# Optimization experiments

Hardware: AMD Instinct MI355X
Metric: run time of the kernel (lower is better)

The kernel has to match this reference:

```python
import jax, jax.numpy as jnp
import numpy as np

ROT_DIM = 32  # rotary sub-dimension hardcoded in the original module


def apply_rope(x, rope):
    # x: [B, T, H, hd], rope: [T, ROT_DIM//2, 2]
    T = x.shape[1]
    rc = rope[:T][:, None]            # [T, 1, 16, 2]
    cos, sin = rc[..., 0], rc[..., 1]  # [T, 1, 16]
    x_rot, x_pass = x[..., :ROT_DIM], x[..., ROT_DIM:]
    x1, x2 = x_rot[..., :ROT_DIM // 2], x_rot[..., ROT_DIM // 2:]
    return jnp.concatenate([x1 * cos - x2 * sin, x2 * cos + x1 * sin, x_pass], axis=-1)


def setup_inputs() -> dict:
    key = jax.random.key(0)
    ks = jax.random.split(key, 6)
    B, T, C, H = 4, 1024, 2048, 32
    hd = C // H
    x = jax.random.normal(ks[0], (B, T, C), dtype=jnp.float32)
    mask = jnp.tril(jnp.ones((T, T), dtype=bool))  # causal, True = attend
    index = jnp.arange(T, dtype=jnp.int64) if jax.config.jax_enable_x64 else jnp.arange(T, dtype=jnp.int32)
    # realistic rotary cos/sin cache
    inv_freq = 1.0 / (10000.0 ** (np.arange(0, ROT_DIM, 2, dtype=np.float32) / ROT_DIM))
    ang = np.arange(T, dtype=np.float32)[:, None] * inv_freq[None, :]  # [T, 16]
    rope = jnp.asarray(np.stack([np.cos(ang), np.sin(ang)], axis=-1))   # [T, 16, 2]
    s = 1.0 / np.sqrt(C)
    Wqkv_w = jax.random.normal(ks[1], (3 * C, C), dtype=jnp.float32) * s
    Wqkv_b = jax.random.normal(ks[2], (3 * C,), dtype=jnp.float32) * 0.01
    out_w = jax.random.normal(ks[3], (C, C), dtype=jnp.float32) * s
    out_b = jax.random.normal(ks[4], (C,), dtype=jnp.float32) * 0.01
    k_cache = jnp.zeros((B, H, T, hd), dtype=jnp.float32)
    v_cache = jnp.zeros((B, H, T, hd), dtype=jnp.float32)
    return {"x": x, "mask": mask, "index": index, "rope": rope,
            "Wqkv_w": Wqkv_w, "Wqkv_b": Wqkv_b, "out_w": out_w, "out_b": out_b,
            "k_cache": k_cache, "v_cache": v_cache}


def reference(x, mask, index, rope, Wqkv_w, Wqkv_b, out_w, out_b, k_cache, v_cache):
    B, T, C = x.shape
    H = 32
    hd = C // H
    qkv = x @ Wqkv_w.T + Wqkv_b                 # [B, T, 3C]
    q, k, v = jnp.split(qkv, 3, axis=-1)
    q = q.reshape(B, T, H, hd)
    k = k.reshape(B, T, H, hd)
    v = v.reshape(B, T, H, hd)
    q = apply_rope(q, rope)
    k = apply_rope(k, rope)
    q = q.transpose(0, 2, 1, 3)                 # [B, H, T, hd]
    k = k.transpose(0, 2, 1, 3)
    v = v.transpose(0, 2, 1, 3)
    # KV-cache scatter update; index = arange(T) covers the full cache, so the
    # subsequent slice [:, :, :index[-1]+1] is the whole cache (static shape).
    k_full = k_cache.at[:, :, index].set(k)
    v_full = v_cache.at[:, :, index].set(v)
    scores = jnp.einsum('bhqd,bhkd->bhqk', q, k_full) / jnp.sqrt(jnp.asarray(hd, x.dtype))
    scores = jnp.where(mask, scores, jnp.finfo(x.dtype).min)
    attn = jax.nn.softmax(scores, axis=-1)
    ctx = jnp.einsum('bhqk,bhkd->bhqd', attn, v_full)
    ctx = ctx.transpose(0, 2, 1, 3).reshape(B, T, C)
    return ctx @ out_w.T + out_b
```

## Files before the change

kernel.cpp:

```cpp
#include <hip/hip_runtime.h>

typedef unsigned short u16;
typedef unsigned int u32;
typedef __bf16 bf16x8 __attribute__((ext_vector_type(8)));
typedef float floatx4 __attribute__((ext_vector_type(4)));
typedef u16 u16x4 __attribute__((ext_vector_type(4)));
typedef u16 u16x8 __attribute__((ext_vector_type(8)));
typedef u32 u32x2 __attribute__((ext_vector_type(2)));

#define B_ 4
#define T_ 1024
#define C_ 2048
#define H_ 32
#define HD_ 64

__device__ __forceinline__ float b2f(u16 u) {
    u32 x = ((u32)u) << 16;
    return __builtin_bit_cast(float, x);
}
__device__ __forceinline__ u16 f2b(float f) {
    u32 i = __builtin_bit_cast(u32, f);
    u32 r = (i + 0x7FFFu + ((i >> 16) & 1u)) >> 16;
    return (u16)r;
}
__device__ __forceinline__ u32 pack2(float a, float b) {
    const u32 ua = __builtin_bit_cast(u32, a) + 0x8000u;
    const u32 ub = __builtin_bit_cast(u32, b) + 0x8000u;
    return __builtin_amdgcn_perm(ub, ua, 0x07060302u);
}

#define GLOAD16(gp, lp) __builtin_amdgcn_global_load_lds( \
    (const __attribute__((address_space(1))) void*)(gp),  \
    (__attribute__((address_space(3))) void*)(lp), 16, 0, 0)

__global__ __launch_bounds__(256) void convert_bf16(const float* __restrict__ src,
                                                    u16* __restrict__ dst, int n4) {
    const int stride = gridDim.x * 256;
    for (int i = blockIdx.x * 256 + threadIdx.x; i < n4; i += stride) {
        const floatx4 v = *(const floatx4*)(src + (size_t)i * 4);
        const u32x2 h = {pack2(v.x, v.y), pack2(v.z, v.w)};
        *(u32x2*)(dst + (size_t)i * 4) = h;
    }
}

template <int MODE>
__global__ __launch_bounds__(256) void gemm_bt(const u16* __restrict__ A,
                                               const u16* __restrict__ W,
                                               const float* __restrict__ bias,
                                               const float* __restrict__ rope,
                                               void* __restrict__ o0v,
                                               u16* __restrict__ o1,
                                               u16* __restrict__ o2) {
    const int Kdim = 2048;
    __shared__ __align__(16) u16 As[128 * 64];
    __shared__ __align__(16) u16 Bs[128 * 64];

    const int tid = threadIdx.x;
    const int w = tid >> 6, lane = tid & 63;
    const int wr = w >> 1, wc = w & 1;
    const int quad = lane >> 4, l15 = lane & 15;
    const int mBase = blockIdx.y * 128, nBase = blockIdx.x * 128;

    floatx4 acc[4][4] = {};

    const int lrow = lane >> 3;
    const int lcol = ((lane & 7) ^ lrow) * 8;
    const u16* Ap = A + (size_t)(mBase + lrow) * Kdim + lcol;
    const u16* Wp = W + (size_t)(nBase + lrow) * Kdim + lcol;

    const int xk = l15 & 7;

    for (int k0 = 0; k0 < Kdim; k0 += 64) {
#pragma unroll
        for (int i = 0; i < 4; i++) {
            const int c = i * 4 + w;
            GLOAD16(Ap + (size_t)c * 8 * Kdim + k0, &As[c * 512]);
            GLOAD16(Wp + (size_t)c * 8 * Kdim + k0, &Bs[c * 512]);
        }
        __syncthreads();
#pragma unroll
        for (int ks = 0; ks < 64; ks += 32) {
            bf16x8 af[4], bfr[4];
#pragma unroll
            for (int i = 0; i < 4; i++) {
                const int co = (((ks >> 3) + quad) ^ xk) * 8;
                af[i] = *(const bf16x8*)&As[(wr * 64 + i * 16 + l15) * 64 + co];
            }
#pragma unroll
            for (int j = 0; j < 4; j++) {
                const int co = (((ks >> 3) + quad) ^ xk) * 8;
                bfr[j] = *(const bf16x8*)&Bs[(wc * 64 + j * 16 + l15) * 64 + co];
            }
#pragma unroll
            for (int i = 0; i < 4; i++)
#pragma unroll
                for (int j = 0; j < 4; j++)
                    acc[i][j] = __builtin_amdgcn_mfma_f32_16x16x32_bf16(af[i], bfr[j], acc[i][j], 0, 0, 0);
        }
        __syncthreads();
    }

    const int nq = nBase + wc * 64;
    float bv[4];
#pragma unroll
    for (int j = 0; j < 4; j++) bv[j] = bias[nq + j * 16 + l15];

    if (MODE == 0) {
        const int region = nq >> 11;
        const int h = (nq & 2047) >> 6;
        const int d = l15;
        u16* dst = (region == 0) ? (u16*)o0v : ((region == 1) ? o1 : o2);
#pragma unroll
        for (int i = 0; i < 4; i++) {
#pragma unroll
            for (int r = 0; r < 4; r++) {
                const int m = mBase + wr * 64 + i * 16 + quad * 4 + r;
                const int b = m >> 10, t = m & 1023;
                float v0 = acc[i][0][r] + bv[0];
                float v1 = acc[i][1][r] + bv[1];
                float v2 = acc[i][2][r] + bv[2];
                float v3 = acc[i][3][r] + bv[3];
                const size_t base = ((size_t)(b * H_ + h) * T_ + t) * HD_;
                if (region < 2) {
                    const float cz = rope[t * 32 + d * 2];
                    const float sz = rope[t * 32 + d * 2 + 1];
                    const float n0 = v0 * cz - v1 * sz;
                    const float n1 = v1 * cz + v0 * sz;
                    dst[base + d] = f2b(n0);
                    dst[base + 16 + d] = f2b(n1);
                } else {
                    dst[base + d] = f2b(v0);
                    dst[base + 16 + d] = f2b(v1);
                }
                dst[base + 32 + d] = f2b(v2);
                dst[base + 48 + d] = f2b(v3);
            }
        }
    } else {
        float* outf = (float*)o0v;
#pragma unroll
        for (int i = 0; i < 4; i++)
#pragma unroll
            for (int r = 0; r < 4; r++) {
                const int m = mBase + wr * 64 + i * 16 + quad * 4 + r;
                const size_t o = (size_t)m * 2048 + nq;
#pragma unroll
                for (int j = 0; j < 4; j++)
                    outf[o + j * 16 + l15] = acc[i][j][r] + bv[j];
            }
    }
}

#define VT_STR 72

__global__ __launch_bounds__(256) void attn_mfma(const u16* __restrict__ qT,
                                                 const u16* __restrict__ kT,
                                                 const u16* __restrict__ vT,
                                                 u16* __restrict__ ctx) {
    __shared__ __align__(16) u16 Vt[2][64 * VT_STR];
    __shared__ __align__(16) u16 Pt[4 * 16 * VT_STR];

    const int tid = threadIdx.x;
    const int w = tid >> 6, lane = tid & 63;
    const int quad = lane >> 4, l15 = lane & 15;
    const int bh = blockIdx.y;
    const size_t headBase = (size_t)bh * (T_ * HD_);

    u16* myPt = &Pt[w * 16 * VT_STR];
    const int vhd = tid & 63, vkb = tid >> 6;
    const float SC = 0.18033688011112042f;

    int gb = 0;
#pragma unroll 1
    for (int ti = 0; ti < 2; ti++) {
        const int qt = ti ? (15 - (int)blockIdx.x) : (int)blockIdx.x;

        bf16x8 qf[2];
        {
            const u16* qrow = qT + headBase + ((size_t)qt * 64 + w * 16 + l15) * HD_ + quad * 8;
            qf[0] = __builtin_bit_cast(bf16x8, *(const u16x8*)(qrow));
            qf[1] = __builtin_bit_cast(bf16x8, *(const u16x8*)(qrow + 32));
        }

        float m_i = -1e30f, l_i = 0.f;
        floatx4 oacc[4] = {};

        for (int kt = 0; kt <= qt; kt++) {
            const u16* kp = kT + headBase + (size_t)kt * 64 * HD_;
            const u16* vp = vT + headBase + (size_t)kt * 64 * HD_;

            u16 vreg[16];
#pragma unroll
            for (int c = 0; c < 16; c++)
                vreg[c] = vp[(vkb * 16 + c) * HD_ + vhd];

            floatx4 st[4] = {};
#pragma unroll
            for (int mi = 0; mi < 4; mi++) {
                const u16* krow = kp + (mi * 16 + l15) * HD_ + quad * 8;
                const bf16x8 kf0 = __builtin_bit_cast(bf16x8, *(const u16x8*)(krow));
                const bf16x8 kf1 = __builtin_bit_cast(bf16x8, *(const u16x8*)(krow + 32));
                st[mi] = __builtin_amdgcn_mfma_f32_16x16x32_bf16(kf0, qf[0], st[mi], 0, 0, 0);
                st[mi] = __builtin_amdgcn_mfma_f32_16x16x32_bf16(kf1, qf[1], st[mi], 0, 0, 0);
            }

            u16* vt = Vt[gb];
#pragma unroll
            for (int c4 = 0; c4 < 4; c4++) {
                const u16x4 vv = {vreg[c4 * 4], vreg[c4 * 4 + 1], vreg[c4 * 4 + 2], vreg[c4 * 4 + 3]};
                *(u16x4*)&vt[vhd * VT_STR + vkb * 16 + c4 * 4] = vv;
            }
            __syncthreads();

            float pmax = -1e30f;
#pragma unroll
            for (int mi = 0; mi < 4; mi++)
#pragma unroll
                for (int r = 0; r < 4; r++) {
                    float sv = st[mi][r] * SC;
                    if (kt == qt && (mi * 16 + quad * 4 + r) > (w * 16 + l15)) sv = -1e30f;
                    st[mi][r] = sv;
                    pmax = fmaxf(pmax, sv);
                }
            pmax = fmaxf(pmax, __shfl_xor(pmax, 16, 64));
            pmax = fmaxf(pmax, __shfl_xor(pmax, 32, 64));
            const float mnew = fmaxf(m_i, pmax);
            const float alpha = __builtin_amdgcn_exp2f(m_i - mnew);
            m_i = mnew;

            float psum = 0.f;
#pragma unroll
            for (int mi = 0; mi < 4; mi++) {
                float p[4];
#pragma unroll
                for (int r = 0; r < 4; r++) {
                    p[r] = __builtin_amdgcn_exp2f(st[mi][r] - mnew);
                    psum += p[r];
                }
                const u32x2 pk2 = {pack2(p[0], p[1]), pack2(p[2], p[3])};
                *(u32x2*)&myPt[l15 * VT_STR + mi * 16 + quad * 4] = pk2;
            }
            psum += __shfl_xor(psum, 16, 64);
            psum += __shfl_xor(psum, 32, 64);
            l_i = l_i * alpha + psum;

#pragma unroll
            for (int mi = 0; mi < 4; mi++) oacc[mi] *= alpha;

            bf16x8 pf[2];
            pf[0] = __builtin_bit_cast(bf16x8, *(const u16x8*)&myPt[l15 * VT_STR + quad * 8]);
            pf[1] = __builtin_bit_cast(bf16x8, *(const u16x8*)&myPt[l15 * VT_STR + 32 + quad * 8]);
#pragma unroll
            for (int mi = 0; mi < 4; mi++) {
                const bf16x8 vf0 = __builtin_bit_cast(bf16x8, *(const u16x8*)&vt[(mi * 16 + l15) * VT_STR + quad * 8]);
                const bf16x8 vf1 = __builtin_bit_cast(bf16x8, *(const u16x8*)&vt[(mi * 16 + l15) * VT_STR + 32 + quad * 8]);
                oacc[mi] = __builtin_amdgcn_mfma_f32_16x16x32_bf16(vf0, pf[0], oacc[mi], 0, 0, 0);
                oacc[mi] = __builtin_amdgcn_mfma_f32_16x16x32_bf16(vf1, pf[1], oacc[mi], 0, 0, 0);
            }
            gb ^= 1;
        }

        const float inv = 1.0f / l_i;
        const int b = bh >> 5, h = bh & 31;
        const int t = qt * 64 + w * 16 + l15;
        u16* cp = ctx + ((size_t)(b * T_ + t)) * C_ + h * HD_;
#pragma unroll
        for (int mi = 0; mi < 4; mi++) {
            const u16x4 ov = {f2b(oacc[mi][0] * inv), f2b(oacc[mi][1] * inv),
                              f2b(oacc[mi][2] * inv), f2b(oacc[mi][3] * inv)};
            *(u16x4*)(cp + mi * 16 + quad * 4) = ov;
        }
    }
}

extern "C" void kernel_launch(void* const* d_in, const int* in_sizes, int n_in,
                              void* d_out, int out_size, void* d_ws, size_t ws_size,
                              hipStream_t stream) {
    const float* x      = (const float*)d_in[0];
    const float* rope   = (const float*)d_in[3];
    const float* Wqkv_w = (const float*)d_in[4];
    const float* Wqkv_b = (const float*)d_in[5];
    const float* out_w  = (const float*)d_in[6];
    const float* out_b  = (const float*)d_in[7];
    float* out = (float*)d_out;

    const size_t headElems = (size_t)B_ * H_ * T_ * HD_;
    u16* xb    = (u16*)d_ws;
    u16* wqkvb = xb + headElems;
    u16* outwb = wqkvb + 12582912;
    u16* qTp   = outwb + 4194304;
    u16* kTp   = qTp + headElems;
    u16* vTp   = kTp + headElems;
    u16* ctx   = xb;

    convert_bf16<<<dim3(2048), 256, 0, stream>>>(x, xb, 2097152);
    convert_bf16<<<dim3(3072), 256, 0, stream>>>(Wqkv_w, wqkvb, 3145728);
    convert_bf16<<<dim3(1024), 256, 0, stream>>>(out_w, outwb, 1048576);

    gemm_bt<0><<<dim3(48, 32), 256, 0, stream>>>(xb, wqkvb, Wqkv_b, rope, qTp, kTp, vTp);
    attn_mfma<<<dim3(8, 128), 256, 0, stream>>>(qTp, kTp, vTp, ctx);
    gemm_bt<1><<<dim3(16, 32), 256, 0, stream>>>(ctx, outwb, out_b, rope, out, nullptr, nullptr);
}
```

Baseline: 433.6 us.

## Replace QKV GEMM with 256x256 double-buffered 8-wave pipelined kernel

Adds a new QKV projection kernel that uses 256x256 output tiles with 512 threads and double-buffered LDS staging. Global-to-LDS loads are interleaved with MFMA phases, guarded by explicit barriers, waitcnts and setprio, and blocks are remapped with a swizzle for L2 locality. Bias, rope and the head-split layout are kept in the epilogue. The aim is more data reuse per tile and overlap of memory with compute. In exchange it uses much more LDS (128KB) and registers, so occupancy drops, and the 384-block grid may leave the 256 CUs unevenly loaded.

```diff
diff --git a/kernel.cpp b/kernel.cpp
--- a/kernel.cpp
+++ b/kernel.cpp
@@ -33,6 +33,13 @@
     (const __attribute__((address_space(1))) void*)(gp),  \
     (__attribute__((address_space(3))) void*)(lp), 16, 0, 0)
 
+#define BAR()   __builtin_amdgcn_s_barrier()
+#define LGKM0() asm volatile("s_waitcnt lgkmcnt(0)" ::: "memory")
+#define VMW(n)  asm volatile("s_waitcnt vmcnt(" #n ")" ::: "memory")
+#define PRIO1() __builtin_amdgcn_s_setprio(1)
+#define PRIO0() __builtin_amdgcn_s_setprio(0)
+#define MFMA(a, b, c) __builtin_amdgcn_mfma_f32_16x16x32_bf16(a, b, c, 0, 0, 0)
+
 __global__ __launch_bounds__(256) void convert_bf16(const float* __restrict__ src,
                                                     u16* __restrict__ dst, int n4) {
     const int stride = gridDim.x * 256;
@@ -40,6 +47,169 @@
         const floatx4 v = *(const floatx4*)(src + (size_t)i * 4);
         const u32x2 h = {pack2(v.x, v.y), pack2(v.z, v.w)};
         *(u32x2*)(dst + (size_t)i * 4) = h;
+    }
+}
+
+#define HALFSTEP(BUF, STG, TS, VMN)                                           \
+  {                                                                           \
+    const u16* as = &As[BUF][0];                                              \
+    const u16* bs = &Bs[BUF][0];                                              \
+    u16* asw = &As[BUF][0];                                                   \
+    u16* bsw = &Bs[BUF][0];                                                   \
+    const u16* Apt = Abase + (size_t)(TS) * 64;                               \
+    const u16* Wpt = Wbase + (size_t)(TS) * 64;                               \
+    bf16x8 afr[4][2], bfr[4][2];                                              \
+                            \
+    _Pragma("unroll") for (int i = 0; i < 4; i++) {                           \
+      afr[i][0] = *(const bf16x8*)&as[aro + i * 1024 + co0];                  \
+      afr[i][1] = *(const bf16x8*)&as[aro + i * 1024 + co1];                  \
+    }                                                                         \
+    _Pragma("unroll") for (int j = 0; j < 2; j++) {                           \
+      bfr[j][0] = *(const bf16x8*)&bs[bro + j * 1024 + co0];                  \
+      bfr[j][1] = *(const bf16x8*)&bs[bro + j * 1024 + co1];                  \
+    }                                                                         \
+    BAR(); LGKM0(); PRIO1();                                                  \
+    _Pragma("unroll") for (int i = 0; i < 4; i++)                             \
+      _Pragma("unroll") for (int j = 0; j < 2; j++) {                         \
+        acc[i][j] = MFMA(afr[i][0], bfr[j][0], acc[i][j]);                    \
+        acc[i][j] = MFMA(afr[i][1], bfr[j][1], acc[i][j]);                    \
+      }                                                                       \
+    PRIO0(); BAR();                                                           \
+                 \
+    _Pragma("unroll") for (int j = 2; j < 4; j++) {                           \
+      bfr[j][0] = *(const bf16x8*)&bs[bro + j * 1024 + co0];                  \
+      bfr[j][1] = *(const bf16x8*)&bs[bro + j * 1024 + co1];                  \
+    }                                                                         \
+    if (STG) {                                                                \
+      GLOAD16(Apt, &asw[(w * 8) * 64]);                                       \
+      GLOAD16(Apt + (size_t)2 * 131072, &asw[(128 + w * 8) * 64]);            \
+    }                                                                         \
+    BAR(); LGKM0(); PRIO1();                                                  \
+    _Pragma("unroll") for (int i = 0; i < 4; i++)                             \
+      _Pragma("unroll") for (int j = 2; j < 4; j++) {                         \
+        acc[i][j] = MFMA(afr[i][0], bfr[j][0], acc[i][j]);                    \
+        acc[i][j] = MFMA(afr[i][1], bfr[j][1], acc[i][j]);                    \
+      }                                                                       \
+    PRIO0(); BAR();                                                           \
+                       \
+    _Pragma("unroll") for (int i = 0; i < 4; i++) {                           \
+      afr[i][0] = *(const bf16x8*)&as[aro + 4096 + i * 1024 + co0];           \
+      afr[i][1] = *(const bf16x8*)&as[aro + 4096 + i * 1024 + co1];           \
+    }                                                                         \
+    if (STG) {                                                                \
+      GLOAD16(Wpt, &bsw[(w * 8) * 64]);                                       \
+      GLOAD16(Wpt + (size_t)131072, &bsw[(64 + w * 8) * 64]);                 \
+    }                                                                         \
+    BAR(); LGKM0(); PRIO1();                                                  \
+    _Pragma("unroll") for (int i = 0; i < 4; i++)                             \
+      _Pragma("unroll") for (int j = 0; j < 2; j++) {                         \
+        acc[4 + i][j] = MFMA(afr[i][0], bfr[j][0], acc[4 + i][j]);            \
+        acc[4 + i][j] = MFMA(afr[i][1], bfr[j][1], acc[4 + i][j]);            \
+      }                                                                       \
+    PRIO0(); BAR();                                                           \
+            \
+    if (STG) {                                                                \
+      GLOAD16(Wpt + (size_t)2 * 131072, &bsw[(128 + w * 8) * 64]);            \
+      GLOAD16(Wpt + (size_t)3 * 131072, &bsw[(192 + w * 8) * 64]);            \
+      GLOAD16(Apt + (size_t)131072, &asw[(64 + w * 8) * 64]);                 \
+      GLOAD16(Apt + (size_t)3 * 131072, &asw[(192 + w * 8) * 64]);            \
+    }                                                                         \
+    BAR(); PRIO1();                                                           \
+    _Pragma("unroll") for (int i = 0; i < 4; i++)                             \
+      _Pragma("unroll") for (int j = 2; j < 4; j++) {                         \
+        acc[4 + i][j] = MFMA(afr[i][0], bfr[j][0], acc[4 + i][j]);            \
+        acc[4 + i][j] = MFMA(afr[i][1], bfr[j][1], acc[4 + i][j]);            \
+      }                                                                       \
+    PRIO0(); VMW(VMN); BAR();                                                 \
+  }
+
+__global__ __launch_bounds__(512) void gemm256_qkv(const u16* __restrict__ A,
+                                                   const u16* __restrict__ W,
+                                                   const float* __restrict__ bias,
+                                                   const float* __restrict__ rope,
+                                                   u16* __restrict__ oq,
+                                                   u16* __restrict__ ok,
+                                                   u16* __restrict__ ov) {
+    __shared__ __align__(16) u16 As[2][256 * 64];
+    __shared__ __align__(16) u16 Bs[2][256 * 64];
+
+    const int tid = threadIdx.x;
+    const int w = tid >> 6, lane = tid & 63;
+    const int quad = lane >> 4, l15 = lane & 15;
+    const int wr = w >> 2, wc = w & 3;
+
+    const int lin = blockIdx.y * 24 + blockIdx.x;
+    const int swz = (lin & 7) * 48 + (lin >> 3);
+    const int mBase = (swz & 15) * 256;
+    const int nBase = (swz >> 4) * 256;
+
+    const int srow = w * 8 + (lane >> 3);
+    const int scol = ((lane & 7) ^ (lane >> 3)) * 8;
+    const u16* Abase = A + (size_t)(mBase + srow) * 2048 + scol;
+    const u16* Wbase = W + (size_t)(nBase + srow) * 2048 + scol;
+
+    const int xk = l15 & 7;
+    const int co0 = ((0 * 4 + quad) ^ xk) * 8;
+    const int co1 = ((1 * 4 + quad) ^ xk) * 8;
+    const int aro = (wr * 128 + l15) * 64;
+    const int bro = (wc * 64 + l15) * 64;
+
+    floatx4 acc[8][4] = {};
+
+#pragma unroll
+    for (int u = 0; u < 4; u++) {
+        GLOAD16(Abase + (size_t)u * 131072, &As[0][(u * 64 + w * 8) * 64]);
+        GLOAD16(Wbase + (size_t)u * 131072, &Bs[0][(u * 64 + w * 8) * 64]);
+    }
+#pragma unroll
+    for (int u = 0; u < 4; u++) {
+        GLOAD16(Abase + (size_t)u * 131072 + 64, &As[1][(u * 64 + w * 8) * 64]);
+        GLOAD16(Wbase + (size_t)u * 131072 + 64, &Bs[1][(u * 64 + w * 8) * 64]);
+    }
+    VMW(8);
+    BAR();
+
+#pragma unroll 1
+    for (int t = 0; t < 30; t += 2) {
+        HALFSTEP(0, 1, t + 2, 8)
+        HALFSTEP(1, 1, t + 3, 8)
+    }
+    HALFSTEP(0, 0, 0, 0)
+    HALFSTEP(1, 0, 0, 0)
+
+    const int nq = nBase + wc * 64;
+    float bv[4];
+#pragma unroll
+    for (int j = 0; j < 4; j++) bv[j] = bias[nq + j * 16 + l15];
+    const int region = nq >> 11;
+    const int hh = (nq & 2047) >> 6;
+    const int d = l15;
+    u16* dst = (region == 0) ? oq : ((region == 1) ? ok : ov);
+#pragma unroll
+    for (int mi = 0; mi < 8; mi++) {
+#pragma unroll
+        for (int r = 0; r < 4; r++) {
+            const int m = mBase + wr * 128 + mi * 16 + quad * 4 + r;
+            const int bb = m >> 10, tt = m & 1023;
+            float v0 = acc[mi][0][r] + bv[0];
+            float v1 = acc[mi][1][r] + bv[1];
+            float v2 = acc[mi][2][r] + bv[2];
+            float v3 = acc[mi][3][r] + bv[3];
+            const size_t base = ((size_t)(bb * H_ + hh) * T_ + tt) * HD_;
+            if (region < 2) {
+                const float cz = rope[tt * 32 + d * 2];
+                const float sz = rope[tt * 32 + d * 2 + 1];
+                const float n0 = v0 * cz - v1 * sz;
+                const float n1 = v1 * cz + v0 * sz;
+                dst[base + d] = f2b(n0);
+                dst[base + 16 + d] = f2b(n1);
+            } else {
+                dst[base + d] = f2b(v0);
+                dst[base + 16 + d] = f2b(v1);
+            }
+            dst[base + 32 + d] = f2b(v2);
+            dst[base + 48 + d] = f2b(v3);
+        }
     }
 }
 
@@ -297,7 +467,7 @@
     convert_bf16<<<dim3(3072), 256, 0, stream>>>(Wqkv_w, wqkvb, 3145728);
     convert_bf16<<<dim3(1024), 256, 0, stream>>>(out_w, outwb, 1048576);
 
-    gemm_bt<0><<<dim3(48, 32), 256, 0, stream>>>(xb, wqkvb, Wqkv_b, rope, qTp, kTp, vTp);
+    gemm256_qkv<<<dim3(24, 16), 512, 0, stream>>>(xb, wqkvb, Wqkv_b, rope, qTp, kTp, vTp);
     attn_mfma<<<dim3(8, 128), 256, 0, stream>>>(qTp, kTp, vTp, ctx);
     gemm_bt<1><<<dim3(16, 32), 256, 0, stream>>>(ctx, outwb, out_b, rope, out, nullptr, nullptr);
 }
```

New measurement: 464.2 us. +7.0%, slower.

## Process two key tiles per softmax step in attention and fuse conversion kernels

Applied to the files above, without the earlier changes.

The attention loop now handles 128 keys per iteration (two 64-key tiles) with a single online-softmax update. This halves the per-iteration rescale, reductions and barriers, at the cost of a single-buffered V tile with an extra barrier, larger LDS strides and more registers for eight score fragments. The three fp32-to-bf16 conversion launches are also merged into one kernel that picks its source by index range, which removes launch overhead. The contiguous workspace layout lets a single destination pointer be used.

```diff
diff --git a/kernel.cpp b/kernel.cpp
--- a/kernel.cpp
+++ b/kernel.cpp
@@ -33,11 +33,18 @@
     (const __attribute__((address_space(1))) void*)(gp),  \
     (__attribute__((address_space(3))) void*)(lp), 16, 0, 0)
 
-__global__ __launch_bounds__(256) void convert_bf16(const float* __restrict__ src,
-                                                    u16* __restrict__ dst, int n4) {
+__global__ __launch_bounds__(256) void convert_all(const float* __restrict__ x,
+                                                   const float* __restrict__ wqkv,
+                                                   const float* __restrict__ outw,
+                                                   u16* __restrict__ dst) {
     const int stride = gridDim.x * 256;
-    for (int i = blockIdx.x * 256 + threadIdx.x; i < n4; i += stride) {
-        const floatx4 v = *(const floatx4*)(src + (size_t)i * 4);
+    for (int i = blockIdx.x * 256 + threadIdx.x; i < 6291456; i += stride) {
+        const float* s;
+        int off;
+        if (i < 2097152) { s = x; off = i; }
+        else if (i < 5242880) { s = wqkv; off = i - 2097152; }
+        else { s = outw; off = i - 5242880; }
+        const floatx4 v = *(const floatx4*)(s + (size_t)off * 4);
         const u32x2 h = {pack2(v.x, v.y), pack2(v.z, v.w)};
         *(u32x2*)(dst + (size_t)i * 4) = h;
     }
@@ -151,13 +158,13 @@
     }
 }
 
-#define VT_STR 72
+#define VT_STR 136
 
 __global__ __launch_bounds__(256) void attn_mfma(const u16* __restrict__ qT,
                                                  const u16* __restrict__ kT,
                                                  const u16* __restrict__ vT,
                                                  u16* __restrict__ ctx) {
-    __shared__ __align__(16) u16 Vt[2][64 * VT_STR];
+    __shared__ __align__(16) u16 Vt[64 * VT_STR];
     __shared__ __align__(16) u16 Pt[4 * 16 * VT_STR];
 
     const int tid = threadIdx.x;
@@ -170,33 +177,40 @@
     const int vhd = tid & 63, vkb = tid >> 6;
     const float SC = 0.18033688011112042f;
 
-    int gb = 0;
 #pragma unroll 1
     for (int ti = 0; ti < 2; ti++) {
         const int qt = ti ? (15 - (int)blockIdx.x) : (int)blockIdx.x;
+        const int qtb = qt * 64;
+        const int qrow = w * 16 + l15;
 
         bf16x8 qf[2];
         {
-            const u16* qrow = qT + headBase + ((size_t)qt * 64 + w * 16 + l15) * HD_ + quad * 8;
-            qf[0] = __builtin_bit_cast(bf16x8, *(const u16x8*)(qrow));
-            qf[1] = __builtin_bit_cast(bf16x8, *(const u16x8*)(qrow + 32));
+            const u16* qr = qT + headBase + (size_t)(qtb + qrow) * HD_ + quad * 8;
+            qf[0] = __builtin_bit_cast(bf16x8, *(const u16x8*)(qr));
+            qf[1] = __builtin_bit_cast(bf16x8, *(const u16x8*)(qr + 32));
         }
 
         float m_i = -1e30f, l_i = 0.f;
         floatx4 oacc[4] = {};
-
-        for (int kt = 0; kt <= qt; kt++) {
-            const u16* kp = kT + headBase + (size_t)kt * 64 * HD_;
-            const u16* vp = vT + headBase + (size_t)kt * 64 * HD_;
+        const int niter = (qt + 2) >> 1;
+
+#pragma unroll 1
+        for (int kt = 0; kt < niter; kt++) {
+            const int kb0 = kt * 128;
+            const int v1 = (kb0 + 64 <= qtb);
+            const u16* kp = kT + headBase + (size_t)kb0 * HD_;
+            const u16* vp = vT + headBase + (size_t)kb0 * HD_;
+
+            floatx4 st[8];
 
             u16 vreg[16];
 #pragma unroll
             for (int c = 0; c < 16; c++)
                 vreg[c] = vp[(vkb * 16 + c) * HD_ + vhd];
 
-            floatx4 st[4] = {};
 #pragma unroll
             for (int mi = 0; mi < 4; mi++) {
+                st[mi] = floatx4{};
                 const u16* krow = kp + (mi * 16 + l15) * HD_ + quad * 8;
                 const bf16x8 kf0 = __builtin_bit_cast(bf16x8, *(const u16x8*)(krow));
                 const bf16x8 kf1 = __builtin_bit_cast(bf16x8, *(const u16x8*)(krow + 32));
@@ -204,24 +218,52 @@
                 st[mi] = __builtin_amdgcn_mfma_f32_16x16x32_bf16(kf1, qf[1], st[mi], 0, 0, 0);
             }
 
-            u16* vt = Vt[gb];
+            __syncthreads();
+
 #pragma unroll
             for (int c4 = 0; c4 < 4; c4++) {
                 const u16x4 vv = {vreg[c4 * 4], vreg[c4 * 4 + 1], vreg[c4 * 4 + 2], vreg[c4 * 4 + 3]};
-                *(u16x4*)&vt[vhd * VT_STR + vkb * 16 + c4 * 4] = vv;
-            }
+                *(u16x4*)&Vt[vhd * VT_STR + vkb * 16 + c4 * 4] = vv;
+            }
+
+            if (v1) {
+#pragma unroll
+                for (int c = 0; c < 16; c++)
+                    vreg[c] = vp[(64 + vkb * 16 + c) * HD_ + vhd];
+#pragma unroll
+                for (int mi = 0; mi < 4; mi++) {
+                    st[4 + mi] = floatx4{};
+                    const u16* krow = kp + (64 + mi * 16 + l15) * HD_ + quad * 8;
+                    const bf16x8 kf0 = __builtin_bit_cast(bf16x8, *(const u16x8*)(krow));
+                    const bf16x8 kf1 = __builtin_bit_cast(bf16x8, *(const u16x8*)(krow + 32));
+                    st[4 + mi] = __builtin_amdgcn_mfma_f32_16x16x32_bf16(kf0, qf[0], st[4 + mi], 0, 0, 0);
+                    st[4 + mi] = __builtin_amdgcn_mfma_f32_16x16x32_bf16(kf1, qf[1], st[4 + mi], 0, 0, 0);
+                }
+#pragma unroll
+                for (int c4 = 0; c4 < 4; c4++) {
+                    const u16x4 vv = {vreg[c4 * 4], vreg[c4 * 4 + 1], vreg[c4 * 4 + 2], vreg[c4 * 4 + 3]};
+                    *(u16x4*)&Vt[vhd * VT_STR + 64 + vkb * 16 + c4 * 4] = vv;
+                }
+            }
+
             __syncthreads();
 
+            const int nmi = v1 ? 8 : 4;
+
             float pmax = -1e30f;
 #pragma unroll
-            for (int mi = 0; mi < 4; mi++)
+            for (int s = 0; s < 8; s++) {
+                if (s >= nmi) break;
+                const int hb = kb0 + (s >> 2) * 64;
+                const int diag = (hb == qtb);
 #pragma unroll
                 for (int r = 0; r < 4; r++) {
-                    float sv = st[mi][r] * SC;
-                    if (kt == qt && (mi * 16 + quad * 4 + r) > (w * 16 + l15)) sv = -1e30f;
-                    st[mi][r] = sv;
+                    float sv = st[s][r] * SC;
+                    if (diag && ((s & 3) * 16 + quad * 4 + r) > qrow) sv = -1e30f;
+                    st[s][r] = sv;
                     pmax = fmaxf(pmax, sv);
                 }
+            }
             pmax = fmaxf(pmax, __shfl_xor(pmax, 16, 64));
             pmax = fmaxf(pmax, __shfl_xor(pmax, 32, 64));
             const float mnew = fmaxf(m_i, pmax);
@@ -230,15 +272,16 @@
 
             float psum = 0.f;
 #pragma unroll
-            for (int mi = 0; mi < 4; mi++) {
+            for (int s = 0; s < 8; s++) {
+                if (s >= nmi) break;
                 float p[4];
 #pragma unroll
                 for (int r = 0; r < 4; r++) {
-                    p[r] = __builtin_amdgcn_exp2f(st[mi][r] - mnew);
+                    p[r] = __builtin_amdgcn_exp2f(st[s][r] - mnew);
                     psum += p[r];
                 }
                 const u32x2 pk2 = {pack2(p[0], p[1]), pack2(p[2], p[3])};
-                *(u32x2*)&myPt[l15 * VT_STR + mi * 16 + quad * 4] = pk2;
+                *(u32x2*)&myPt[l15 * VT_STR + s * 16 + quad * 4] = pk2;
             }
             psum += __shfl_xor(psum, 16, 64);
             psum += __shfl_xor(psum, 32, 64);
@@ -247,22 +290,22 @@
 #pragma unroll
             for (int mi = 0; mi < 4; mi++) oacc[mi] *= alpha;
 
-            bf16x8 pf[2];
-            pf[0] = __builtin_bit_cast(bf16x8, *(const u16x8*)&myPt[l15 * VT_STR + quad * 8]);
-            pf[1] = __builtin_bit_cast(bf16x8, *(const u16x8*)&myPt[l15 * VT_STR + 32 + quad * 8]);
-#pragma unroll
-            for (int mi = 0; mi < 4; mi++) {
-                const bf16x8 vf0 = __builtin_bit_cast(bf16x8, *(const u16x8*)&vt[(mi * 16 + l15) * VT_STR + quad * 8]);
-                const bf16x8 vf1 = __builtin_bit_cast(bf16x8, *(const u16x8*)&vt[(mi * 16 + l15) * VT_STR + 32 + quad * 8]);
-                oacc[mi] = __builtin_amdgcn_mfma_f32_16x16x32_bf16(vf0, pf[0], oacc[mi], 0, 0, 0);
-                oacc[mi] = __builtin_amdgcn_mfma_f32_16x16x32_bf16(vf1, pf[1], oacc[mi], 0, 0, 0);
-            }
-            gb ^= 1;
+            const int nks = v1 ? 4 : 2;
+#pragma unroll
+            for (int ks = 0; ks < 4; ks++) {
+                if (ks >= nks) break;
+                const bf16x8 pf = __builtin_bit_cast(bf16x8, *(const u16x8*)&myPt[l15 * VT_STR + ks * 32 + quad * 8]);
+#pragma unroll
+                for (int mi = 0; mi < 4; mi++) {
+                    const bf16x8 vf = __builtin_bit_cast(bf16x8, *(const u16x8*)&Vt[(mi * 16 + l15) * VT_STR + ks * 32 + quad * 8]);
+                    oacc[mi] = __builtin_amdgcn_mfma_f32_16x16x32_bf16(vf, pf, oacc[mi], 0, 0, 0);
+                }
+            }
         }
 
         const float inv = 1.0f / l_i;
         const int b = bh >> 5, h = bh & 31;
-        const int t = qt * 64 + w * 16 + l15;
+        const int t = qtb + qrow;
         u16* cp = ctx + ((size_t)(b * T_ + t)) * C_ + h * HD_;
 #pragma unroll
         for (int mi = 0; mi < 4; mi++) {
@@ -293,9 +336,7 @@
     u16* vTp   = kTp + headElems;
     u16* ctx   = xb;
 
-    convert_bf16<<<dim3(2048), 256, 0, stream>>>(x, xb, 2097152);
-    convert_bf16<<<dim3(3072), 256, 0, stream>>>(Wqkv_w, wqkvb, 3145728);
-    convert_bf16<<<dim3(1024), 256, 0, stream>>>(out_w, outwb, 1048576);
+    convert_all<<<dim3(3072), 256, 0, stream>>>(x, Wqkv_w, out_w, xb);
 
     gemm_bt<0><<<dim3(48, 32), 256, 0, stream>>>(xb, wqkvb, Wqkv_b, rope, qTp, kTp, vTp);
     attn_mfma<<<dim3(8, 128), 256, 0, stream>>>(qTp, kTp, vTp, ctx);
```

New measurement: 445.3 us. 2.7% more time.

## Prefetch K tiles into registers, lazy softmax rescale, merge conversion kernels

Applied to the files above, without the earlier changes.

The attention inner loop is unrolled by two, with K fragments for the next tile loaded into alternating register buffers while the current tile is processed. This hides global-load latency. Online-softmax rescaling of the accumulators is skipped unless the running max grows past a threshold, which removes exp and multiply work. The three fp32-to-bf16 conversion launches are merged into one kernel. Register pressure rises from the double-buffered K fragments, and the launch bounds now request higher occupancy, so spilling is a risk.

```diff
diff --git a/kernel.cpp b/kernel.cpp
--- a/kernel.cpp
+++ b/kernel.cpp
@@ -33,11 +33,18 @@
     (const __attribute__((address_space(1))) void*)(gp),  \
     (__attribute__((address_space(3))) void*)(lp), 16, 0, 0)
 
-__global__ __launch_bounds__(256) void convert_bf16(const float* __restrict__ src,
-                                                    u16* __restrict__ dst, int n4) {
+__global__ __launch_bounds__(256) void convert_all(const float* __restrict__ x,
+                                                   const float* __restrict__ wqkv,
+                                                   const float* __restrict__ outw,
+                                                   u16* __restrict__ dst) {
     const int stride = gridDim.x * 256;
-    for (int i = blockIdx.x * 256 + threadIdx.x; i < n4; i += stride) {
-        const floatx4 v = *(const floatx4*)(src + (size_t)i * 4);
+    for (int i = blockIdx.x * 256 + threadIdx.x; i < 6291456; i += stride) {
+        const float* s;
+        int off;
+        if (i < 2097152) { s = x; off = i; }
+        else if (i < 5242880) { s = wqkv; off = i - 2097152; }
+        else { s = outw; off = i - 5242880; }
+        const floatx4 v = *(const floatx4*)(s + (size_t)off * 4);
         const u32x2 h = {pack2(v.x, v.y), pack2(v.z, v.w)};
         *(u32x2*)(dst + (size_t)i * 4) = h;
     }
@@ -153,10 +160,83 @@
 
 #define VT_STR 72
 
-__global__ __launch_bounds__(256) void attn_mfma(const u16* __restrict__ qT,
-                                                 const u16* __restrict__ kT,
-                                                 const u16* __restrict__ vT,
-                                                 u16* __restrict__ ctx) {
+#define LOADK(DST, KT)                                                         \
+  {                                                                            \
+    const u16* kp_ = kbase + (size_t)(KT) * 64 * HD_;                          \
+    _Pragma("unroll") for (int mi = 0; mi < 4; mi++) {                         \
+      const u16* kr_ = kp_ + (mi * 16 + l15) * HD_ + quad * 8;                 \
+      DST[2 * mi]     = __builtin_bit_cast(bf16x8, *(const u16x8*)(kr_));      \
+      DST[2 * mi + 1] = __builtin_bit_cast(bf16x8, *(const u16x8*)(kr_ + 32)); \
+    }                                                                          \
+  }
+
+#define STEP(KT, KC, KN)                                                       \
+  {                                                                            \
+    const u16* vp_ = vT + headBase + (size_t)(KT) * 64 * HD_;                  \
+    u16 vreg[16];                                                              \
+    _Pragma("unroll") for (int c = 0; c < 16; c++)                             \
+        vreg[c] = vp_[(vkb * 16 + c) * HD_ + vhd];                             \
+    if ((KT) < qt) LOADK(KN, (KT) + 1)                                         \
+    floatx4 st[4];                                                             \
+    _Pragma("unroll") for (int mi = 0; mi < 4; mi++) {                         \
+      st[mi] = floatx4{};                                                      \
+      st[mi] = __builtin_amdgcn_mfma_f32_16x16x32_bf16(KC[2 * mi], qf[0], st[mi], 0, 0, 0);     \
+      st[mi] = __builtin_amdgcn_mfma_f32_16x16x32_bf16(KC[2 * mi + 1], qf[1], st[mi], 0, 0, 0); \
+    }                                                                          \
+    u16* vt = Vt[gb];                                                          \
+    _Pragma("unroll") for (int c4 = 0; c4 < 4; c4++) {                         \
+      const u16x4 vv = {vreg[c4 * 4], vreg[c4 * 4 + 1], vreg[c4 * 4 + 2], vreg[c4 * 4 + 3]};    \
+      *(u16x4*)&vt[vhd * VT_STR + vkb * 16 + c4 * 4] = vv;                     \
+    }                                                                          \
+    __syncthreads();                                                           \
+    float pmax = -1e30f;                                                       \
+    const int diag_ = ((KT) == qt);                                            \
+    _Pragma("unroll") for (int mi = 0; mi < 4; mi++)                           \
+      _Pragma("unroll") for (int r = 0; r < 4; r++) {                          \
+        float sv = st[mi][r] * SC;                                             \
+        if (diag_ && (mi * 16 + quad * 4 + r) > qrow) sv = -1e30f;             \
+        st[mi][r] = sv;                                                        \
+        pmax = fmaxf(pmax, sv);                                                \
+      }                                                                        \
+    pmax = fmaxf(pmax, __shfl_xor(pmax, 16, 64));                              \
+    pmax = fmaxf(pmax, __shfl_xor(pmax, 32, 64));                              \
+    const bool resc_ = !__all(pmax <= m_i + 11.0f);                            \
+    float mnew = m_i;                                                          \
+    if (resc_) {                                                               \
+      mnew = fmaxf(m_i, pmax);                                                 \
+      const float alpha_ = __builtin_amdgcn_exp2f(m_i - mnew);                 \
+      m_i = mnew;                                                              \
+      l_i *= alpha_;                                                           \
+      _Pragma("unroll") for (int mi = 0; mi < 4; mi++) oacc[mi] *= alpha_;     \
+    }                                                                          \
+    float psum = 0.f;                                                          \
+    _Pragma("unroll") for (int mi = 0; mi < 4; mi++) {                         \
+      float p0 = __builtin_amdgcn_exp2f(st[mi][0] - mnew);                     \
+      float p1 = __builtin_amdgcn_exp2f(st[mi][1] - mnew);                     \
+      float p2 = __builtin_amdgcn_exp2f(st[mi][2] - mnew);                     \
+      float p3 = __builtin_amdgcn_exp2f(st[mi][3] - mnew);                     \
+      psum += p0 + p1 + p2 + p3;                                               \
+      const u32x2 pk2 = {pack2(p0, p1), pack2(p2, p3)};                        \
+      *(u32x2*)&myPt[l15 * VT_STR + mi * 16 + quad * 4] = pk2;                 \
+    }                                                                          \
+    psum += __shfl_xor(psum, 16, 64);                                          \
+    psum += __shfl_xor(psum, 32, 64);                                          \
+    l_i += psum;                                                               \
+    bf16x8 pf0 = __builtin_bit_cast(bf16x8, *(const u16x8*)&myPt[l15 * VT_STR + quad * 8]);     \
+    bf16x8 pf1 = __builtin_bit_cast(bf16x8, *(const u16x8*)&myPt[l15 * VT_STR + 32 + quad * 8]);\
+    _Pragma("unroll") for (int mi = 0; mi < 4; mi++) {                         \
+      const bf16x8 vf0 = __builtin_bit_cast(bf16x8, *(const u16x8*)&vt[(mi * 16 + l15) * VT_STR + quad * 8]);      \
+      const bf16x8 vf1 = __builtin_bit_cast(bf16x8, *(const u16x8*)&vt[(mi * 16 + l15) * VT_STR + 32 + quad * 8]); \
+      oacc[mi] = __builtin_amdgcn_mfma_f32_16x16x32_bf16(vf0, pf0, oacc[mi], 0, 0, 0);          \
+      oacc[mi] = __builtin_amdgcn_mfma_f32_16x16x32_bf16(vf1, pf1, oacc[mi], 0, 0, 0);          \
+    }                                                                          \
+    gb ^= 1;                                                                   \
+  }
+
+__global__ __launch_bounds__(256, 4) void attn_mfma(const u16* __restrict__ qT,
+                                                    const u16* __restrict__ kT,
+                                                    const u16* __restrict__ vT,
+                                                    u16* __restrict__ ctx) {
     __shared__ __align__(16) u16 Vt[2][64 * VT_STR];
     __shared__ __align__(16) u16 Pt[4 * 16 * VT_STR];
 
@@ -169,100 +249,39 @@
     u16* myPt = &Pt[w * 16 * VT_STR];
     const int vhd = tid & 63, vkb = tid >> 6;
     const float SC = 0.18033688011112042f;
+    const u16* kbase = kT + headBase;
 
     int gb = 0;
 #pragma unroll 1
     for (int ti = 0; ti < 2; ti++) {
         const int qt = ti ? (15 - (int)blockIdx.x) : (int)blockIdx.x;
+        const int qrow = w * 16 + l15;
 
         bf16x8 qf[2];
         {
-            const u16* qrow = qT + headBase + ((size_t)qt * 64 + w * 16 + l15) * HD_ + quad * 8;
-            qf[0] = __builtin_bit_cast(bf16x8, *(const u16x8*)(qrow));
-            qf[1] = __builtin_bit_cast(bf16x8, *(const u16x8*)(qrow + 32));
+            const u16* qr = qT + headBase + ((size_t)qt * 64 + qrow) * HD_ + quad * 8;
+            qf[0] = __builtin_bit_cast(bf16x8, *(const u16x8*)(qr));
+            qf[1] = __builtin_bit_cast(bf16x8, *(const u16x8*)(qr + 32));
         }
 
         float m_i = -1e30f, l_i = 0.f;
         floatx4 oacc[4] = {};
 
-        for (int kt = 0; kt <= qt; kt++) {
-            const u16* kp = kT + headBase + (size_t)kt * 64 * HD_;
-            const u16* vp = vT + headBase + (size_t)kt * 64 * HD_;
-
-            u16 vreg[16];
-#pragma unroll
-            for (int c = 0; c < 16; c++)
-                vreg[c] = vp[(vkb * 16 + c) * HD_ + vhd];
-
-            floatx4 st[4] = {};
-#pragma unroll
-            for (int mi = 0; mi < 4; mi++) {
-                const u16* krow = kp + (mi * 16 + l15) * HD_ + quad * 8;
-                const bf16x8 kf0 = __builtin_bit_cast(bf16x8, *(const u16x8*)(krow));
-                const bf16x8 kf1 = __builtin_bit_cast(bf16x8, *(const u16x8*)(krow + 32));
-                st[mi] = __builtin_amdgcn_mfma_f32_16x16x32_bf16(kf0, qf[0], st[mi], 0, 0, 0);
-                st[mi] = __builtin_amdgcn_mfma_f32_16x16x32_bf16(kf1, qf[1], st[mi], 0, 0, 0);
-            }
-
-            u16* vt = Vt[gb];
-#pragma unroll
-            for (int c4 = 0; c4 < 4; c4++) {
-                const u16x4 vv = {vreg[c4 * 4], vreg[c4 * 4 + 1], vreg[c4 * 4 + 2], vreg[c4 * 4 + 3]};
-                *(u16x4*)&vt[vhd * VT_STR + vkb * 16 + c4 * 4] = vv;
-            }
-            __syncthreads();
-
-            float pmax = -1e30f;
-#pragma unroll
-            for (int mi = 0; mi < 4; mi++)
-#pragma unroll
-                for (int r = 0; r < 4; r++) {
-                    float sv = st[mi][r] * SC;
-                    if (kt == qt && (mi * 16 + quad * 4 + r) > (w * 16 + l15)) sv = -1e30f;
-                    st[mi][r] = sv;
-                    pmax = fmaxf(pmax, sv);
-                }
-            pmax = fmaxf(pmax, __shfl_xor(pmax, 16, 64));
-            pmax = fmaxf(pmax, __shfl_xor(pmax, 32, 64));
-            const float mnew = fmaxf(m_i, pmax);
-            const float alpha = __builtin_amdgcn_exp2f(m_i - mnew);
-            m_i = mnew;
-
-            float psum = 0.f;
-#pragma unroll
-            for (int mi = 0; mi < 4; mi++) {
-                float p[4];
-#pragma unroll
-                for (int r = 0; r < 4; r++) {
-                    p[r] = __builtin_amdgcn_exp2f(st[mi][r] - mnew);
-                    psum += p[r];
-                }
-                const u32x2 pk2 = {pack2(p[0], p[1]), pack2(p[2], p[3])};
-                *(u32x2*)&myPt[l15 * VT_STR + mi * 16 + quad * 4] = pk2;
-            }
-            psum += __shfl_xor(psum, 16, 64);
-            psum += __shfl_xor(psum, 32, 64);
-            l_i = l_i * alpha + psum;
-
-#pragma unroll
-            for (int mi = 0; mi < 4; mi++) oacc[mi] *= alpha;
-
-            bf16x8 pf[2];
-            pf[0] = __builtin_bit_cast(bf16x8, *(const u16x8*)&myPt[l15 * VT_STR + quad * 8]);
-            pf[1] = __builtin_bit_cast(bf16x8, *(const u16x8*)&myPt[l15 * VT_STR + 32 + quad * 8]);
-#pragma unroll
-            for (int mi = 0; mi < 4; mi++) {
-                const bf16x8 vf0 = __builtin_bit_cast(bf16x8, *(const u16x8*)&vt[(mi * 16 + l15) * VT_STR + quad * 8]);
-                const bf16x8 vf1 = __builtin_bit_cast(bf16x8, *(const u16x8*)&vt[(mi * 16 + l15) * VT_STR + 32 + quad * 8]);
-                oacc[mi] = __builtin_amdgcn_mfma_f32_16x16x32_bf16(vf0, pf[0], oacc[mi], 0, 0, 0);
-                oacc[mi] = __builtin_amdgcn_mfma_f32_16x16x32_bf16(vf1, pf[1], oacc[mi], 0, 0, 0);
-            }
-            gb ^= 1;
-        }
+        bf16x8 kA[8], kB[8];
+        LOADK(kA, 0)
+
+        int kt = 0;
+#pragma unroll 1
+        while (kt + 2 <= qt + 1) {
+            STEP(kt, kA, kB)
+            STEP(kt + 1, kB, kA)
+            kt += 2;
+        }
+        if (kt <= qt) STEP(kt, kA, kB)
 
         const float inv = 1.0f / l_i;
         const int b = bh >> 5, h = bh & 31;
-        const int t = qt * 64 + w * 16 + l15;
+        const int t = qt * 64 + qrow;
         u16* cp = ctx + ((size_t)(b * T_ + t)) * C_ + h * HD_;
 #pragma unroll
         for (int mi = 0; mi < 4; mi++) {
@@ -293,9 +312,7 @@
     u16* vTp   = kTp + headElems;
     u16* ctx   = xb;
 
-    convert_bf16<<<dim3(2048), 256, 0, stream>>>(x, xb, 2097152);
-    convert_bf16<<<dim3(3072), 256, 0, stream>>>(Wqkv_w, wqkvb, 3145728);
-    convert_bf16<<<dim3(1024), 256, 0, stream>>>(out_w, outwb, 1048576);
+    convert_all<<<dim3(3072), 256, 0, stream>>>(x, Wqkv_w, out_w, xb);
 
     gemm_bt<0><<<dim3(48, 32), 256, 0, stream>>>(xb, wqkvb, Wqkv_b, rope, qTp, kTp, vTp);
     attn_mfma<<<dim3(8, 128), 256, 0, stream>>>(qTp, kTp, vTp, ctx);
```

New measurement: 480.3 us. +10.8%, slower.
